# Kernel optimization log

Hardware: AMD Instinct MI355X
Metric: run time of the kernel (lower is better)

The kernel has to match this reference:

```python
import jax, jax.numpy as jnp
import numpy as np

E = 1024   # embed_dim
H = 16     # num_heads
NQ = 8     # ffn_dim == n_qubits
B, S = 2, 2048


def setup_inputs() -> dict:
    key = jax.random.key(0)
    ks = jax.random.split(key, 8)
    g = lambda k, sh, sc=1.0: jax.random.normal(k, sh, jnp.float32) * sc
    return {
        "x": g(ks[0], (B, S, E)),
        "w_qkv": g(ks[1], (3 * E, E), 0.02),      # nn.Linear(E, 3E, bias=False).weight
        "w_comb": g(ks[2], (E, E), 0.02),          # combine Linear weight
        "b_comb": jnp.zeros((E,), jnp.float32),
        "gamma1": jnp.ones((E,), jnp.float32),     # norm1
        "beta1": jnp.zeros((E,), jnp.float32),
        "gamma2": jnp.ones((E,), jnp.float32),     # norm2
        "beta2": jnp.zeros((E,), jnp.float32),
        "theta": g(ks[3], (NQ,)),                  # trainable RY angles
        "w1": g(ks[4], (1, NQ), 0.3),              # linear1 weight [1, n_qubits]
        "b1": jnp.zeros((1,), jnp.float32),
    }


def _layernorm(x, g, b, eps=1e-5):
    m = jnp.mean(x, axis=-1, keepdims=True)
    v = jnp.var(x, axis=-1, keepdims=True)
    return (x - m) * jax.lax.rsqrt(v + eps) * g + b


def reference(x, w_qkv, w_comb, b_comb, gamma1, beta1, gamma2, beta2, theta, w1, b1):
    Bx, Sx, Em = x.shape
    dk = Em // H
    # ---- attention ----
    qkv = (x @ w_qkv.T).reshape(Bx, Sx, 3, H, dk)
    q = jnp.transpose(qkv[:, :, 0], (0, 2, 1, 3))  # [B,H,S,dk]
    k = jnp.transpose(qkv[:, :, 1], (0, 2, 1, 3))
    v = jnp.transpose(qkv[:, :, 2], (0, 2, 1, 3))
    scores = jnp.einsum('bhqd,bhkd->bhqk', q, k) / jnp.sqrt(jnp.float32(dk))
    probs = jax.nn.softmax(scores, axis=-1)        # dropout = identity (eval)
    out = jnp.einsum('bhqk,bhkd->bhqd', probs, v)
    out = jnp.transpose(out, (0, 2, 1, 3)).reshape(Bx, Sx, Em)
    attn = out @ w_comb.T + b_comb
    x1 = _layernorm(x + attn, gamma1, beta1)
    # ---- quantum FFN: RX(x_i) encode, RY(theta_i), <Z_i> = cos(theta_i)*cos(x_i) ----
    z = jnp.cos(x1[..., :theta.shape[0]]) * jnp.cos(theta)  # [B,S,NQ]
    ffn = z @ w1.T + b1                                      # [B,S,1], broadcasts
    return _layernorm(x1 + ffn, gamma2, beta2)
```

## Files before the change

kernel.cpp:

```cpp
#include <hip/hip_runtime.h>
#include <hip/hip_bf16.h>
#include <math.h>

typedef __bf16 bf16;
typedef bf16 bf16x8 __attribute__((ext_vector_type(8)));
typedef bf16 bf16x4 __attribute__((ext_vector_type(4)));
typedef float f32x4 __attribute__((ext_vector_type(4)));
typedef unsigned int u32;

#define EMB 1024
#define NH 16
#define DK 64
#define SEQ 2048
#define NB 2
#define NTOK (NB*SEQ)

#define QSCALE 0.18033688011112043f

#if defined(__has_builtin)
#if __has_builtin(__builtin_amdgcn_exp2f)
#define EXP2(x) __builtin_amdgcn_exp2f(x)
#else
#define EXP2(x) exp2f(x)
#endif
#else
#define EXP2(x) exp2f(x)
#endif

__device__ __forceinline__ void gl_lds16(const void* g, void* l) {
    __builtin_amdgcn_global_load_lds(
        (const __attribute__((address_space(1))) u32*)g,
        (__attribute__((address_space(3))) u32*)l, 16, 0, 0);
}

#define SWZ(row, colblk) (((row)*64) + ((((colblk) ^ ((row)&7)))*8))

#define PSTR 72

__device__ __forceinline__ void xcd_remap(int gx, int* bx, int* by) {
    int gy  = gridDim.y;
    int nwg = gx * gy;
    int wg  = *by * gx + *bx;
    int per = nwg >> 3;
    int s   = (wg & 7) * per + (wg >> 3);
    *bx = s % gx;
    *by = s / gx;
}

__global__ __launch_bounds__(256) void convert3(
    const float* __restrict__ s0, const float* __restrict__ s1,
    const float* __restrict__ s2,
    bf16* __restrict__ d0, bf16* __restrict__ d1, bf16* __restrict__ d2)
{
    const float* src; bf16* dst; int n;
    switch (blockIdx.y) {
        case 0:  src = s0; dst = d0; n = NTOK*EMB;  break;
        case 1:  src = s1; dst = d1; n = 3*EMB*EMB; break;
        default: src = s2; dst = d2; n = EMB*EMB;   break;
    }
    int i = (blockIdx.x * 256 + threadIdx.x) * 8;
    if (i + 7 < n) {
        float4 a = *(const float4*)(src + i);
        float4 b = *(const float4*)(src + i + 4);
        bf16x8 o;
        o[0] = (bf16)a.x; o[1] = (bf16)a.y; o[2] = (bf16)a.z; o[3] = (bf16)a.w;
        o[4] = (bf16)b.x; o[5] = (bf16)b.y; o[6] = (bf16)b.z; o[7] = (bf16)b.w;
        *(bf16x8*)(dst + i) = o;
    }
}

template<int MODE, int BM>
__global__ __launch_bounds__(256) void gemm_bt(
    const bf16* __restrict__ Aa, const bf16* __restrict__ Bb,
    bf16* __restrict__ qb, bf16* __restrict__ kb, bf16* __restrict__ vtb,
    float* __restrict__ outc, int Kdim)
{
    constexpr int MI = BM / 32;
    __shared__ __align__(16) bf16 At[BM*64];
    __shared__ __align__(16) bf16 Bt[128*64];
    const int tid  = threadIdx.x;
    const int w    = tid >> 6, lane = tid & 63;
    const int quad = lane >> 4, l15 = lane & 15;
    const int wr   = w >> 1,   wc  = w & 1;
    int bx = blockIdx.x, by = blockIdx.y;
    xcd_remap(gridDim.x, &bx, &by);
    const int m0 = by * BM, n0 = bx * 128;
    const int lrow = lane >> 3;
    const int lswz = ((lane & 7) ^ lrow) * 8;

    f32x4 acc[MI][4] = {};

    for (int k0 = 0; k0 < Kdim; k0 += 64) {
        __syncthreads();
        for (int i = 0; i < MI; ++i) {
            int r = w*(BM/4) + i*8 + lrow;
            gl_lds16(Aa + (size_t)(m0 + r)*Kdim + k0 + lswz, At + (w*(BM/4) + i*8)*64);
        }
        for (int i = 0; i < 4; ++i) {
            int r = w*32 + i*8 + lrow;
            gl_lds16(Bb + (size_t)(n0 + r)*Kdim + k0 + lswz, Bt + (w*32 + i*8)*64);
        }
        __syncthreads();
        for (int kk = 0; kk < 2; ++kk) {
            bf16x8 a[MI], b[4];
            for (int i = 0; i < MI; ++i) {
                int row = wr*(BM/2) + i*16 + l15;
                a[i] = *(const bf16x8*)(At + SWZ(row, 4*kk + quad));
            }
            for (int j = 0; j < 4; ++j) {
                int row = wc*64 + j*16 + l15;
                b[j] = *(const bf16x8*)(Bt + SWZ(row, 4*kk + quad));
            }
            __builtin_amdgcn_s_setprio(1);
            for (int i = 0; i < MI; ++i)
                for (int j = 0; j < 4; ++j)
                    acc[i][j] = __builtin_amdgcn_mfma_f32_16x16x32_bf16(a[i], b[j], acc[i][j], 0, 0, 0);
            __builtin_amdgcn_s_setprio(0);
        }
    }

    for (int i = 0; i < MI; ++i) for (int j = 0; j < 4; ++j) {
        int rb  = m0 + wr*(BM/2) + i*16 + quad*4;
        int col = n0 + wc*64 + j*16 + l15;
        if (MODE == 0) {
            int c = col >> 10, h = (col >> 6) & 15, d = col & 63;
            int b_ = rb >> 11, s = rb & 2047;
            int bh = b_*NH + h;
            if (c == 2) {
                bf16 tmp[4] __attribute__((aligned(8)));
                for (int r = 0; r < 4; ++r) tmp[r] = (bf16)acc[i][j][r];
                *(ushort4*)(vtb + ((size_t)bh*DK + d)*SEQ + s) = *(ushort4*)tmp;
            } else if (c == 0) {
                for (int r = 0; r < 4; ++r)
                    qb[((size_t)bh*SEQ + s + r)*DK + d] = (bf16)(acc[i][j][r] * QSCALE);
            } else {
                for (int r = 0; r < 4; ++r)
                    kb[((size_t)bh*SEQ + s + r)*DK + d] = (bf16)acc[i][j][r];
            }
        } else {
            for (int r = 0; r < 4; ++r)
                outc[(size_t)(rb + r)*EMB + col] = acc[i][j][r];
        }
    }
}

__global__ __launch_bounds__(512) void attn_kernel(
    const bf16* __restrict__ q, const bf16* __restrict__ k,
    const bf16* __restrict__ vt, bf16* __restrict__ out)
{
    __shared__ __align__(16) bf16 QP[8*16*PSTR];
    __shared__ __align__(16) bf16 Kt0[64*64];
    __shared__ __align__(16) bf16 Kt1[64*64];
    __shared__ __align__(16) bf16 Vt0[64*64];
    __shared__ __align__(16) bf16 Vt1[64*64];

    const int tid  = threadIdx.x;
    const int w    = tid >> 6, lane = tid & 63;
    const int quad = lane >> 4, l15 = lane & 15;
    int qt = blockIdx.x, bh = blockIdx.y;
    xcd_remap(gridDim.x, &qt, &bh);
    const int lrow = lane >> 3;
    const int lswz = ((lane & 7) ^ lrow) * 8;

    for (int i = 0; i < 2; ++i) {
        int r = w*16 + i*8 + lrow;
        gl_lds16(q + ((size_t)bh*SEQ + qt*128 + r)*DK + lswz, QP + (w*16 + i*8)*64);
    }
    asm volatile("s_waitcnt vmcnt(0)" ::: "memory");

    bf16x8 qf[2];
    for (int kk = 0; kk < 2; ++kk)
        qf[kk] = *(const bf16x8*)(QP + SWZ(w*16 + l15, 4*kk + quad));

    bf16* Pw = QP + w * 16 * PSTR;

    f32x4 O[4] = {};
    float psum = 0.f;

    auto stage_kv = [&](int kt, bf16* Kb, bf16* Vb) {
        int r = w*8 + lrow;
        gl_lds16(k  + ((size_t)bh*SEQ + kt*64 + r)*DK + lswz, Kb + (w*8)*64);
        gl_lds16(vt + ((size_t)bh*DK + r)*SEQ + kt*64 + lswz, Vb + (w*8)*64);
    };

    auto compute = [&](const bf16* Kb, const bf16* Vb) {
        f32x4 sc[4] = {};
        for (int kk = 0; kk < 2; ++kk) {
            bf16x8 kf[4];
            for (int j = 0; j < 4; ++j)
                kf[j] = *(const bf16x8*)(Kb + SWZ(j*16 + l15, 4*kk + quad));
            __builtin_amdgcn_s_setprio(1);
            for (int j = 0; j < 4; ++j)
                sc[j] = __builtin_amdgcn_mfma_f32_16x16x32_bf16(kf[j], qf[kk], sc[j], 0, 0, 0);
            __builtin_amdgcn_s_setprio(0);
        }
        for (int j = 0; j < 4; ++j) {
            bf16x4 pk;
            for (int r = 0; r < 4; ++r) {
                float p = EXP2(sc[j][r]);
                psum += p;
                pk[r] = (bf16)p;
            }
            *(bf16x4*)(Pw + l15*PSTR + j*16 + quad*4) = pk;
        }
        asm volatile("s_waitcnt lgkmcnt(0)" ::: "memory");
        for (int kk = 0; kk < 2; ++kk) {
            bf16x8 vb[4];
            for (int j = 0; j < 4; ++j)
                vb[j] = *(const bf16x8*)(Vb + SWZ(j*16 + l15, 4*kk + quad));
            bf16x8 a = *(const bf16x8*)(Pw + l15*PSTR + kk*32 + quad*8);
            __builtin_amdgcn_s_setprio(1);
            for (int j = 0; j < 4; ++j)
                O[j] = __builtin_amdgcn_mfma_f32_16x16x32_bf16(a, vb[j], O[j], 0, 0, 0);
            __builtin_amdgcn_s_setprio(0);
        }
    };

    stage_kv(0, Kt0, Vt0);
    for (int kt2 = 0; kt2 < SEQ/128; ++kt2) {
        __syncthreads();
        stage_kv(2*kt2 + 1, Kt1, Vt1);
        compute(Kt0, Vt0);
        __syncthreads();
        if (kt2 + 1 < SEQ/128)
            stage_kv(2*kt2 + 2, Kt0, Vt0);
        compute(Kt1, Vt1);
    }

    float s = psum;
    s += __shfl_xor(s, 16, 64);
    s += __shfl_xor(s, 32, 64);
    float inv[4];
    for (int r = 0; r < 4; ++r)
        inv[r] = 1.f / __shfl(s, quad*4 + r, 64);

    const int b_ = bh >> 4, h = bh & 15;
    for (int j = 0; j < 4; ++j)
        for (int r = 0; r < 4; ++r) {
            int t   = b_*SEQ + qt*128 + w*16 + quad*4 + r;
            int col = h*DK + j*16 + l15;
            out[(size_t)t*EMB + col] = (bf16)(O[j][r] * inv[r]);
        }
}

__global__ __launch_bounds__(256) void ln_kernel(
    const float* __restrict__ x, const float* __restrict__ comb,
    const float* __restrict__ bcomb,
    const float* __restrict__ g1, const float* __restrict__ be1,
    const float* __restrict__ g2, const float* __restrict__ be2,
    const float* __restrict__ theta, const float* __restrict__ w1v,
    const float* __restrict__ b1v, float* __restrict__ out)
{
    const int w    = threadIdx.x >> 6, lane = threadIdx.x & 63;
    const int t    = blockIdx.x * 4 + w;

    float r[4][4];
    float s = 0.f, ss = 0.f;
    #pragma unroll
    for (int c = 0; c < 4; ++c) {
        int e = c*256 + lane*4;
        float4 xv = *(const float4*)(x    + (size_t)t*EMB + e);
        float4 cv = *(const float4*)(comb + (size_t)t*EMB + e);
        float4 bv = *(const float4*)(bcomb + e);
        r[c][0] = xv.x + cv.x + bv.x; r[c][1] = xv.y + cv.y + bv.y;
        r[c][2] = xv.z + cv.z + bv.z; r[c][3] = xv.w + cv.w + bv.w;
        #pragma unroll
        for (int i = 0; i < 4; ++i) { s += r[c][i]; ss += r[c][i]*r[c][i]; }
    }
    #pragma unroll
    for (int m = 1; m < 64; m <<= 1) { s += __shfl_xor(s, m, 64); ss += __shfl_xor(ss, m, 64); }
    float mean = s * (1.f/1024.f);
    float var  = ss * (1.f/1024.f) - mean*mean;
    float inv  = rsqrtf(var + 1e-5f);

    float x1[4][4];
    #pragma unroll
    for (int c = 0; c < 4; ++c) {
        int e = c*256 + lane*4;
        #pragma unroll
        for (int i = 0; i < 4; ++i)
            x1[c][i] = (r[c][i] - mean)*inv*g1[e+i] + be1[e+i];
    }

    float pf = 0.f;
    if (lane < 2) {
        #pragma unroll
        for (int i = 0; i < 4; ++i) {
            int e = lane*4 + i;
            pf += cosf(x1[0][i]) * cosf(theta[e]) * w1v[e];
        }
    }
    pf += __shfl_xor(pf, 1, 64);
    float f = __shfl(pf, 0, 64) + b1v[0];

    float s2 = 0.f, ss2 = 0.f;
    #pragma unroll
    for (int c = 0; c < 4; ++c)
        #pragma unroll
        for (int i = 0; i < 4; ++i) {
            float v2 = x1[c][i] + f; s2 += v2; ss2 += v2*v2;
        }
    #pragma unroll
    for (int m = 1; m < 64; m <<= 1) { s2 += __shfl_xor(s2, m, 64); ss2 += __shfl_xor(ss2, m, 64); }
    float mean2 = s2 * (1.f/1024.f);
    float var2  = ss2 * (1.f/1024.f) - mean2*mean2;
    float inv2  = rsqrtf(var2 + 1e-5f);

    #pragma unroll
    for (int c = 0; c < 4; ++c) {
        int e = c*256 + lane*4;
        float4 ov;
        ov.x = ((x1[c][0] + f) - mean2)*inv2*g2[e+0] + be2[e+0];
        ov.y = ((x1[c][1] + f) - mean2)*inv2*g2[e+1] + be2[e+1];
        ov.z = ((x1[c][2] + f) - mean2)*inv2*g2[e+2] + be2[e+2];
        ov.w = ((x1[c][3] + f) - mean2)*inv2*g2[e+3] + be2[e+3];
        *(float4*)(out + (size_t)t*EMB + e) = ov;
    }
}

extern "C" void kernel_launch(void* const* d_in, const int* in_sizes, int n_in,
                              void* d_out, int out_size, void* d_ws, size_t ws_size,
                              hipStream_t stream)
{
    const float* x      = (const float*)d_in[0];
    const float* w_qkv  = (const float*)d_in[1];
    const float* w_comb = (const float*)d_in[2];
    const float* b_comb = (const float*)d_in[3];
    const float* g1     = (const float*)d_in[4];
    const float* be1    = (const float*)d_in[5];
    const float* g2     = (const float*)d_in[6];
    const float* be2    = (const float*)d_in[7];
    const float* theta  = (const float*)d_in[8];
    const float* w1v    = (const float*)d_in[9];
    const float* b1v    = (const float*)d_in[10];
    float* out = (float*)d_out;

    char* ws = (char*)d_ws;
    bf16*  xb     = (bf16*)(ws);
    bf16*  wqkvb  = (bf16*)(ws + ( 8u<<20));
    bf16*  wcombb = (bf16*)(ws + (14u<<20));
    bf16*  qb     = (bf16*)(ws + (16u<<20));
    bf16*  kb     = (bf16*)(ws + (24u<<20));
    bf16*  vtb    = (bf16*)(ws + (32u<<20));
    bf16*  attn   = (bf16*)(ws + (40u<<20));
    float* comb   = (float*)(ws + (16u<<20));

    convert3<<<dim3(2048, 3), 256, 0, stream>>>(x, w_qkv, w_comb, xb, wqkvb, wcombb);

    gemm_bt<0,128><<<dim3(3*EMB/128, NTOK/128), 256, 0, stream>>>(
        xb, wqkvb, qb, kb, vtb, nullptr, EMB);
    attn_kernel<<<dim3(SEQ/128, NB*NH), 512, 0, stream>>>(qb, kb, vtb, attn);
    gemm_bt<1,64><<<dim3(EMB/128, NTOK/64), 256, 0, stream>>>(
        attn, wcombb, nullptr, nullptr, nullptr, comb, EMB);
    ln_kernel<<<NTOK/4, 256, 0, stream>>>(x, comb, b_comb, g1, be1, g2, be2,
                                          theta, w1v, b1v, out);
}
```

Measured before the change: 198.9 us.

## Keep softmax probabilities in registers via permlane32 swap instead of LDS round-trip

The attention inner loop no longer writes the exponentiated score tile to shared memory and reads it back as the A operand of the PV MFMA. Instead it packs the probabilities with v_cvt_pk_bf16_f32 and rearranges them across lanes with permlane32_swap. The V fragments are reloaded as 4-element halves in a permuted column order so the k-index matches the new P layout. This removes LDS stores, reads and a waitcnt per tile, at the cost of more, smaller LDS reads for V and reliance on the operand-layout reasoning being correct.

```diff
diff --git a/kernel.cpp b/kernel.cpp
--- a/kernel.cpp
+++ b/kernel.cpp
@@ -35,8 +35,6 @@
 
 #define SWZ(row, colblk) (((row)*64) + ((((colblk) ^ ((row)&7)))*8))
 
-#define PSTR 72
-
 __device__ __forceinline__ void xcd_remap(int gx, int* bx, int* by) {
     int gy  = gridDim.y;
     int nwg = gx * gy;
@@ -45,6 +43,26 @@
     int s   = (wg & 7) * per + (wg >> 3);
     *bx = s % gx;
     *by = s / gx;
+}
+
+__device__ __forceinline__ u32 cvtpk(float a, float b) {
+    u32 r;
+    asm("v_cvt_pk_bf16_f32 %0, %1, %2" : "=v"(r) : "v"(a), "v"(b));
+    return r;
+}
+
+typedef unsigned u32x2v __attribute__((ext_vector_type(2)));
+__device__ __forceinline__ void plswap(u32 x, u32 y, u32* ox, u32* oy) {
+#if defined(__has_builtin) && __has_builtin(__builtin_amdgcn_permlane32_swap)
+    u32x2v r = __builtin_amdgcn_permlane32_swap(x, y, false, false);
+    *ox = r.x; *oy = r.y;
+#else
+    u32 xs = (u32)__shfl_xor((int)x, 32, 64);
+    u32 ys = (u32)__shfl_xor((int)y, 32, 64);
+    bool hi = (threadIdx.x & 32) != 0;
+    *ox = hi ? ys : x;
+    *oy = hi ? y : xs;
+#endif
 }
 
 __global__ __launch_bounds__(256) void convert3(
@@ -148,7 +166,7 @@
     const bf16* __restrict__ q, const bf16* __restrict__ k,
     const bf16* __restrict__ vt, bf16* __restrict__ out)
 {
-    __shared__ __align__(16) bf16 QP[8*16*PSTR];
+    __shared__ __align__(16) bf16 QP[8*16*64];
     __shared__ __align__(16) bf16 Kt0[64*64];
     __shared__ __align__(16) bf16 Kt1[64*64];
     __shared__ __align__(16) bf16 Vt0[64*64];
@@ -172,8 +190,6 @@
     for (int kk = 0; kk < 2; ++kk)
         qf[kk] = *(const bf16x8*)(QP + SWZ(w*16 + l15, 4*kk + quad));
 
-    bf16* Pw = QP + w * 16 * PSTR;
-
     f32x4 O[4] = {};
     float psum = 0.f;
 
@@ -187,33 +203,54 @@
         f32x4 sc[4] = {};
         for (int kk = 0; kk < 2; ++kk) {
             bf16x8 kf[4];
+            #pragma unroll
             for (int j = 0; j < 4; ++j)
                 kf[j] = *(const bf16x8*)(Kb + SWZ(j*16 + l15, 4*kk + quad));
             __builtin_amdgcn_s_setprio(1);
+            #pragma unroll
             for (int j = 0; j < 4; ++j)
                 sc[j] = __builtin_amdgcn_mfma_f32_16x16x32_bf16(kf[j], qf[kk], sc[j], 0, 0, 0);
             __builtin_amdgcn_s_setprio(0);
         }
+        bf16x4 vb[2][4][2];
+        #pragma unroll
+        for (int kk = 0; kk < 2; ++kk)
+            #pragma unroll
+            for (int j = 0; j < 4; ++j)
+                #pragma unroll
+                for (int a = 0; a < 2; ++a) {
+                    int row = j*16 + l15;
+                    int cb  = (quad >> 1)*4 + kk + a*2;
+                    vb[kk][j][a] = *(const bf16x4*)(
+                        Vb + row*64 + ((cb ^ (row & 7))*8) + (quad & 1)*4);
+                }
+        u32 u[4][2];
+        #pragma unroll
         for (int j = 0; j < 4; ++j) {
-            bf16x4 pk;
-            for (int r = 0; r < 4; ++r) {
-                float p = EXP2(sc[j][r]);
-                psum += p;
-                pk[r] = (bf16)p;
-            }
-            *(bf16x4*)(Pw + l15*PSTR + j*16 + quad*4) = pk;
-        }
-        asm volatile("s_waitcnt lgkmcnt(0)" ::: "memory");
-        for (int kk = 0; kk < 2; ++kk) {
-            bf16x8 vb[4];
-            for (int j = 0; j < 4; ++j)
-                vb[j] = *(const bf16x8*)(Vb + SWZ(j*16 + l15, 4*kk + quad));
-            bf16x8 a = *(const bf16x8*)(Pw + l15*PSTR + kk*32 + quad*8);
-            __builtin_amdgcn_s_setprio(1);
-            for (int j = 0; j < 4; ++j)
-                O[j] = __builtin_amdgcn_mfma_f32_16x16x32_bf16(a, vb[j], O[j], 0, 0, 0);
-            __builtin_amdgcn_s_setprio(0);
-        }
+            float p0 = EXP2(sc[j][0]), p1 = EXP2(sc[j][1]),
+                  p2 = EXP2(sc[j][2]), p3 = EXP2(sc[j][3]);
+            psum += (p0 + p1) + (p2 + p3);
+            u[j][0] = cvtpk(p0, p1);
+            u[j][1] = cvtpk(p2, p3);
+        }
+        union { u32 w4[4]; bf16x8 v; } A0, A1;
+        plswap(u[0][0], u[2][0], &A0.w4[0], &A1.w4[0]);
+        plswap(u[0][1], u[2][1], &A0.w4[1], &A1.w4[1]);
+        plswap(u[1][0], u[3][0], &A0.w4[2], &A1.w4[2]);
+        plswap(u[1][1], u[3][1], &A0.w4[3], &A1.w4[3]);
+        union { bf16x4 h[2]; bf16x8 v; } vv;
+        __builtin_amdgcn_s_setprio(1);
+        #pragma unroll
+        for (int j = 0; j < 4; ++j) {
+            vv.h[0] = vb[0][j][0]; vv.h[1] = vb[0][j][1];
+            O[j] = __builtin_amdgcn_mfma_f32_16x16x32_bf16(A0.v, vv.v, O[j], 0, 0, 0);
+        }
+        #pragma unroll
+        for (int j = 0; j < 4; ++j) {
+            vv.h[0] = vb[1][j][0]; vv.h[1] = vb[1][j][1];
+            O[j] = __builtin_amdgcn_mfma_f32_16x16x32_bf16(A1.v, vv.v, O[j], 0, 0, 0);
+        }
+        __builtin_amdgcn_s_setprio(0);
     };
 
     stage_kv(0, Kt0, Vt0);
```

Measured after the change: 204.0 us. 2.6% more time.

## Double-buffer LDS tiles in GEMM to overlap global loads with MFMA

Applied to the files above, without the earlier changes.

Splits the GEMM shared-memory tiles into two ping-pong buffers. The next K tile is prefetched via global-to-LDS loads while MFMAs run on the current one, which hides memory latency behind compute. The K loop is unrolled by two, so it assumes Kdim is a multiple of 128. This doubles LDS use per block, which may reduce occupancy.

```diff
diff --git a/kernel.cpp b/kernel.cpp
--- a/kernel.cpp
+++ b/kernel.cpp
@@ -76,8 +76,10 @@
     float* __restrict__ outc, int Kdim)
 {
     constexpr int MI = BM / 32;
-    __shared__ __align__(16) bf16 At[BM*64];
-    __shared__ __align__(16) bf16 Bt[128*64];
+    __shared__ __align__(16) bf16 At0[BM*64];
+    __shared__ __align__(16) bf16 At1[BM*64];
+    __shared__ __align__(16) bf16 Bt0[128*64];
+    __shared__ __align__(16) bf16 Bt1[128*64];
     const int tid  = threadIdx.x;
     const int w    = tid >> 6, lane = tid & 63;
     const int quad = lane >> 4, l15 = lane & 15;
@@ -90,33 +92,49 @@
 
     f32x4 acc[MI][4] = {};
 
-    for (int k0 = 0; k0 < Kdim; k0 += 64) {
-        __syncthreads();
+    auto stageAB = [&](int k0, bf16* At, bf16* Bt) {
+        #pragma unroll
         for (int i = 0; i < MI; ++i) {
             int r = w*(BM/4) + i*8 + lrow;
             gl_lds16(Aa + (size_t)(m0 + r)*Kdim + k0 + lswz, At + (w*(BM/4) + i*8)*64);
         }
+        #pragma unroll
         for (int i = 0; i < 4; ++i) {
             int r = w*32 + i*8 + lrow;
             gl_lds16(Bb + (size_t)(n0 + r)*Kdim + k0 + lswz, Bt + (w*32 + i*8)*64);
         }
-        __syncthreads();
+    };
+
+    auto computeAB = [&](const bf16* At, const bf16* Bt) {
+        #pragma unroll
         for (int kk = 0; kk < 2; ++kk) {
             bf16x8 a[MI], b[4];
-            for (int i = 0; i < MI; ++i) {
-                int row = wr*(BM/2) + i*16 + l15;
-                a[i] = *(const bf16x8*)(At + SWZ(row, 4*kk + quad));
-            }
-            for (int j = 0; j < 4; ++j) {
-                int row = wc*64 + j*16 + l15;
-                b[j] = *(const bf16x8*)(Bt + SWZ(row, 4*kk + quad));
-            }
+            #pragma unroll
+            for (int i = 0; i < MI; ++i)
+                a[i] = *(const bf16x8*)(At + SWZ(wr*(BM/2) + i*16 + l15, 4*kk + quad));
+            #pragma unroll
+            for (int j = 0; j < 4; ++j)
+                b[j] = *(const bf16x8*)(Bt + SWZ(wc*64 + j*16 + l15, 4*kk + quad));
             __builtin_amdgcn_s_setprio(1);
+            #pragma unroll
             for (int i = 0; i < MI; ++i)
+                #pragma unroll
                 for (int j = 0; j < 4; ++j)
                     acc[i][j] = __builtin_amdgcn_mfma_f32_16x16x32_bf16(a[i], b[j], acc[i][j], 0, 0, 0);
             __builtin_amdgcn_s_setprio(0);
         }
+    };
+
+    const int NT2 = Kdim >> 7;
+    stageAB(0, At0, Bt0);
+    for (int t2 = 0; t2 < NT2; ++t2) {
+        __syncthreads();
+        stageAB(t2*128 + 64, At1, Bt1);
+        computeAB(At0, Bt0);
+        __syncthreads();
+        if (t2 + 1 < NT2)
+            stageAB(t2*128 + 128, At0, Bt0);
+        computeAB(At1, Bt1);
     }
 
     for (int i = 0; i < MI; ++i) for (int j = 0; j < 4; ++j) {
```

New measurement: 197.1 us (median of 4 runs). Within noise of the previous version (-0.9%).
